# Optimization experiments

Measured on AMD Instinct MI355X. Metric: run time of the kernel, lower is better.

Reference implementation:

```python
import jax, jax.numpy as jnp
import numpy as np

P, M, DG, F, H, DH = 2000, 150, 2000, 256, 4, 64
N1, N2 = P + M, P + DG          # adj1 nodes (patient+med), adj2 nodes (patient+diag)
E1, E2, EGP, EGM = 137600, 256000, 64000, 4800
GNN_LAYERS = 2
SA_HID = 128


def setup_inputs() -> dict:
    key = jax.random.key(0)
    ks = jax.random.split(key, 32)
    ri = lambda k, n, hi: jax.random.randint(k, (n,), 0, hi, dtype=jnp.int32)
    rn = lambda k, shape, scale: (jax.random.normal(k, shape, dtype=jnp.float32) * scale)
    inp = {
        'adj1_rows': ri(ks[0], E1, N1), 'adj1_cols': ri(ks[1], E1, N1),
        'adj1_vals': jax.random.uniform(ks[2], (E1,), dtype=jnp.float32),
        'adj2_rows': ri(ks[3], E2, N2), 'adj2_cols': ri(ks[4], E2, N2),
        'adj2_vals': jax.random.uniform(ks[5], (E2,), dtype=jnp.float32),
        'g0_src': ri(ks[6], EGP, P), 'g0_dst': ri(ks[7], EGP, P),
        'g1_src': ri(ks[8], EGP, P), 'g1_dst': ri(ks[9], EGP, P),
        'g2_src': ri(ks[10], EGM, M), 'g2_dst': ri(ks[11], EGM, M),
        'g3_src': ri(ks[12], EGM, M), 'g3_dst': ri(ks[13], EGM, M),
        'keepRate': 1,
        # learned parameters (xavier-ish scales)
        'pEmbed': rn(ks[14], (P, F), 0.05),
        'mEmbed': rn(ks[15], (M, F), 0.05),
        'dEmbed': rn(ks[16], (DG, F), 0.05),
        'gat_W': rn(ks[17], (4, F, H * DH), (2.0 / (F + H * DH)) ** 0.5),
        'gat_al': rn(ks[18], (4, H, DH), 0.1),
        'gat_ar': rn(ks[19], (4, H, DH), 0.1),
        'gat_b': jnp.zeros((4, H * DH), dtype=jnp.float32),
        'sa_W1': rn(ks[20], (H * DH, SA_HID), (2.0 / (H * DH + SA_HID)) ** 0.5),
        'sa_b1': jnp.zeros((SA_HID,), dtype=jnp.float32),
        'sa_W2': rn(ks[21], (SA_HID, 1), 0.1),
        'out_W': rn(ks[22], (2 * F, M), (2.0 / (2 * F + M)) ** 0.5),
        'out_b': jnp.zeros((M,), dtype=jnp.float32),
    }
    return inp


def _spmm(rows, cols, vals, x, n):
    # sparse adj @ x via gather + segment_sum
    return jax.ops.segment_sum(vals[:, None] * x[cols], rows, num_segments=n)


def _seg_softmax(e, seg, n):
    m = jax.ops.segment_max(e, seg, num_segments=n)          # [n, H]
    ex = jnp.exp(e - m[seg])
    s = jax.ops.segment_sum(ex, seg, num_segments=n)
    return ex / (s[seg] + 1e-9)


def _gat(h, W, al, ar, b, src, dst, n):
    # DGL GATConv, feat/attn dropout = 0, negative_slope = 0.2, activation = elu
    feat = (h @ W).reshape(n, H, DH)                          # [n, H, DH]
    el = (feat * al[None]).sum(-1)                            # [n, H]
    er = (feat * ar[None]).sum(-1)
    e = jax.nn.leaky_relu(el[src] + er[dst], negative_slope=0.2)  # [E, H]
    alpha = _seg_softmax(e, dst, n)                           # softmax over in-edges per dst
    out = jax.ops.segment_sum(alpha[:, :, None] * feat[src], dst, num_segments=n)
    out = out + b.reshape(1, H, DH)
    return jax.nn.elu(out).reshape(n, H * DH)


def _sem_att(z, W1, b1, W2):
    # z: [N, K, F]; shared projection; beta over K meta-paths
    w = (jnp.tanh(z @ W1 + b1) @ W2).mean(0)                  # [K, 1]
    beta = jax.nn.softmax(w, axis=0)                          # [K, 1]
    return (beta[None] * z).sum(1)                            # [N, F]


def reference(adj1_rows, adj1_cols, adj1_vals, adj2_rows, adj2_cols, adj2_vals,
              g0_src, g0_dst, g1_src, g1_dst, g2_src, g2_dst, g3_src, g3_dst,
              keepRate, pEmbed, mEmbed, dEmbed, gat_W, gat_al, gat_ar, gat_b,
              sa_W1, sa_b1, sa_W2, out_W, out_b):
    embeds1 = jnp.concatenate([pEmbed, mEmbed], axis=0)       # [N1, F]
    embeds2 = jnp.concatenate([pEmbed, dEmbed], axis=0)       # [N2, F]
    lat1, lat2 = embeds1, embeds2
    acc1 = jnp.zeros_like(embeds1)
    acc2 = jnp.zeros_like(embeds2)
    for _ in range(GNN_LAYERS):
        lat1 = jax.nn.leaky_relu(_spmm(adj1_rows, adj1_cols, adj1_vals, lat1, N1), negative_slope=0.5)
        lat2 = jax.nn.leaky_relu(_spmm(adj2_rows, adj2_cols, adj2_vals, lat2, N2), negative_slope=0.5)
        acc1 = acc1 + lat1
        acc2 = acc2 + lat2
    p1, m_gcn = acc1[:P], acc1[P:]
    p2, d_gcn = acc2[:P], acc2[P:]

    e0 = _gat(p1, gat_W[0], gat_al[0], gat_ar[0], gat_b[0], g0_src, g0_dst, P)
    e1 = _gat(p2, gat_W[1], gat_al[1], gat_ar[1], gat_b[1], g1_src, g1_dst, P)
    e2 = _gat(m_gcn, gat_W[2], gat_al[2], gat_ar[2], gat_b[2], g2_src, g2_dst, M)
    e3 = _gat(m_gcn, gat_W[3], gat_al[3], gat_ar[3], gat_b[3], g3_src, g3_dst, M)

    patient = _sem_att(jnp.stack([e0, e1], axis=1), sa_W1, sa_b1, sa_W2)  # [P, F]
    med = _sem_att(jnp.stack([e2, e3], axis=1), sa_W1, sa_b1, sa_W2)      # [M, F]

    # broadcasted pairwise concat -> ReLU -> Linear -> sum over pairing axis
    pm = jnp.concatenate([
        jnp.broadcast_to(patient[:, None, :], (P, M, F)),
        jnp.broadcast_to(med[None, :, :], (P, M, F)),
    ], axis=-1).reshape(P * M, 2 * F)
    simi = (jax.nn.relu(pm) @ out_W + out_b).reshape(P, M, M)
    simi_pm = simi.sum(axis=1)                                # [P, M]
    return (simi_pm, d_gcn, med, m_gcn, patient)
```

## Files before the change

kernel.cpp:

```cpp
#include <hip/hip_runtime.h>
#include <cmath>
#include <cstdint>

constexpr int P  = 2000, M = 150, DG = 2000, F = 256, H = 4, DH = 64;
constexpr int N1 = P + M;
constexpr int N2 = P + DG;
constexpr int E1 = 137600, E2 = 256000, EGP = 64000, EGM = 4800;
constexpr int SA_HID = 128;

constexpr int HO1 = E1, HO2 = E1 + E2, HO3 = HO2 + EGP, HO4 = HO3 + EGP,
              HO5 = HO4 + EGM, HOE = HO5 + EGM;

constexpr int CAP_A = 160;
constexpr int CAP_G = 96;
constexpr int OVF_CAP = 4096;

__global__ __launch_bounds__(256) void k_build(
    const int* __restrict__ a1r, const int* __restrict__ a1c, const float* __restrict__ a1v,
    const int* __restrict__ a2r, const int* __restrict__ a2c, const float* __restrict__ a2v,
    const int* __restrict__ d0, const int* __restrict__ s0,
    const int* __restrict__ d1, const int* __restrict__ s1,
    const int* __restrict__ d2, const int* __restrict__ s2,
    const int* __restrict__ d3, const int* __restrict__ s3,
    int* cur1, uint2* ell1, int* cur2, uint2* ell2,
    int* cu0, unsigned* eg0, int* cu1, unsigned* eg1,
    int* cu2, unsigned* eg2, int* cu3, unsigned* eg3,
    int* __restrict__ ovf_n, int4* __restrict__ ovf) {
  int tid = blockIdx.x * 256 + threadIdx.x;
  int T = gridDim.x * 256;
  int seg[4], row[4]; unsigned p0[4], p1[4];
#pragma unroll
  for (int u = 0; u < 4; ++u) {
    int i = tid + u * T;
    seg[u] = -1;
    if (i < HOE) {
      if (i < HO1)      { seg[u] = 0; row[u] = a1r[i]; p0[u] = (unsigned)a1c[i]; p1[u] = __float_as_uint(a1v[i]); }
      else if (i < HO2) { int j = i - HO1; seg[u] = 1; row[u] = a2r[j]; p0[u] = (unsigned)a2c[j]; p1[u] = __float_as_uint(a2v[j]); }
      else if (i < HO3) { int j = i - HO2; seg[u] = 2; row[u] = d0[j]; p0[u] = (unsigned)s0[j]; }
      else if (i < HO4) { int j = i - HO3; seg[u] = 3; row[u] = d1[j]; p0[u] = (unsigned)s1[j]; }
      else if (i < HO5) { int j = i - HO4; seg[u] = 4; row[u] = d2[j]; p0[u] = (unsigned)s2[j]; }
      else              { int j = i - HO5; seg[u] = 5; row[u] = d3[j]; p0[u] = (unsigned)s3[j]; }
    }
  }
#pragma unroll
  for (int u = 0; u < 4; ++u) {
    int r = row[u];
    switch (seg[u]) {
      case 0: { int slot = atomicAdd(&cur1[r], 1);
        if (slot < CAP_A) ell1[(size_t)r * CAP_A + slot] = make_uint2(p0[u], p1[u]);
        else { int o = atomicAdd(&ovf_n[0], 1); if (o < OVF_CAP) ovf[0 * OVF_CAP + o] = make_int4(r, (int)p0[u], (int)p1[u], 0); } } break;
      case 1: { int slot = atomicAdd(&cur2[r], 1);
        if (slot < CAP_A) ell2[(size_t)r * CAP_A + slot] = make_uint2(p0[u], p1[u]);
        else { int o = atomicAdd(&ovf_n[1], 1); if (o < OVF_CAP) ovf[1 * OVF_CAP + o] = make_int4(r, (int)p0[u], (int)p1[u], 0); } } break;
      case 2: { int slot = atomicAdd(&cu0[r], 1);
        if (slot < CAP_G) eg0[(size_t)r * CAP_G + slot] = p0[u];
        else { int o = atomicAdd(&ovf_n[2], 1); if (o < OVF_CAP) ovf[2 * OVF_CAP + o] = make_int4(r, (int)p0[u], 0, 0); } } break;
      case 3: { int slot = atomicAdd(&cu1[r], 1);
        if (slot < CAP_G) eg1[(size_t)r * CAP_G + slot] = p0[u];
        else { int o = atomicAdd(&ovf_n[3], 1); if (o < OVF_CAP) ovf[3 * OVF_CAP + o] = make_int4(r, (int)p0[u], 0, 0); } } break;
      case 4: { int slot = atomicAdd(&cu2[r], 1);
        if (slot < CAP_G) eg2[(size_t)r * CAP_G + slot] = p0[u];
        else { int o = atomicAdd(&ovf_n[4], 1); if (o < OVF_CAP) ovf[4 * OVF_CAP + o] = make_int4(r, (int)p0[u], 0, 0); } } break;
      case 5: { int slot = atomicAdd(&cu3[r], 1);
        if (slot < CAP_G) eg3[(size_t)r * CAP_G + slot] = p0[u];
        else { int o = atomicAdd(&ovf_n[5], 1); if (o < OVF_CAP) ovf[5 * OVF_CAP + o] = make_int4(r, (int)p0[u], 0, 0); } } break;
      default: break;
    }
  }
}

template<int LAYER>
__global__ __launch_bounds__(256) void k_spmm(
    const int* __restrict__ cur1, const uint2* __restrict__ ell1,
    const int* __restrict__ cur2, const uint2* __restrict__ ell2,
    const int* __restrict__ ovf_n, const int4* __restrict__ ovf,
    const float* __restrict__ pE, const float* __restrict__ mE, const float* __restrict__ dE,
    float* __restrict__ lat1, float* __restrict__ lat2,
    float* __restrict__ acc1, float* __restrict__ acc2,
    float* __restrict__ out_mgcn, float* __restrict__ out_dgcn) {
  int gw = (blockIdx.x * 256 + threadIdx.x) >> 6;
  if (gw >= N1 + N2) return;
  int lane = threadIdx.x & 63;
  bool g2 = gw >= N1;
  int row = g2 ? gw - N1 : gw;
  const uint2* pe = (g2 ? ell2 : ell1) + (size_t)row * CAP_A;
  const float* latin = g2 ? lat2 : lat1;
  const float* tailE = g2 ? dE : mE;
  int deg = (g2 ? cur2 : cur1)[row];
  int dn = deg < CAP_A ? deg : CAP_A;
  int fo = lane << 2;
  float4 s = {0.f, 0.f, 0.f, 0.f};
  auto fetch = [&](int c) -> float4 {
    const float* b;
    if (LAYER == 1) b = (c < P) ? (pE + (size_t)c * F) : (tailE + (size_t)(c - P) * F);
    else            b = latin + (size_t)c * F;
    return *(const float4*)(b + fo);
  };
  int i = 0;
  for (; i + 8 <= dn; i += 8) {
    uint2 m[8]; float4 a[8];
#pragma unroll
    for (int u = 0; u < 8; ++u) m[u] = pe[i + u];
#pragma unroll
    for (int u = 0; u < 8; ++u) a[u] = fetch((int)m[u].x);
#pragma unroll
    for (int u = 0; u < 8; ++u) {
      float v = __uint_as_float(m[u].y);
      s.x += v * a[u].x; s.y += v * a[u].y; s.z += v * a[u].z; s.w += v * a[u].w;
    }
  }
  for (; i + 4 <= dn; i += 4) {
    uint2 m0 = pe[i], m1 = pe[i + 1], m2 = pe[i + 2], m3 = pe[i + 3];
    float v0 = __uint_as_float(m0.y), v1 = __uint_as_float(m1.y),
          v2 = __uint_as_float(m2.y), v3 = __uint_as_float(m3.y);
    float4 a0 = fetch((int)m0.x), a1 = fetch((int)m1.x),
           a2 = fetch((int)m2.x), a3 = fetch((int)m3.x);
    s.x += v0 * a0.x + v1 * a1.x + v2 * a2.x + v3 * a3.x;
    s.y += v0 * a0.y + v1 * a1.y + v2 * a2.y + v3 * a3.y;
    s.z += v0 * a0.z + v1 * a1.z + v2 * a2.z + v3 * a3.z;
    s.w += v0 * a0.w + v1 * a1.w + v2 * a2.w + v3 * a3.w;
  }
  for (; i < dn; ++i) {
    uint2 m = pe[i];
    float v = __uint_as_float(m.y);
    float4 a = fetch((int)m.x);
    s.x += v * a.x; s.y += v * a.y; s.z += v * a.z; s.w += v * a.w;
  }
  {
    int gi = g2 ? 1 : 0;
    int on = ovf_n[gi];
    if (on > 0) {
      const int4* ol = ovf + gi * OVF_CAP;
      for (int k = 0; k < on; ++k) {
        int4 e = ol[k];
        if (e.x == row) {
          float v = __int_as_float(e.z);
          float4 a = fetch(e.y);
          s.x += v * a.x; s.y += v * a.y; s.z += v * a.z; s.w += v * a.w;
        }
      }
    }
  }
  float4 l;
  l.x = s.x > 0.f ? s.x : 0.5f * s.x;
  l.y = s.y > 0.f ? s.y : 0.5f * s.y;
  l.z = s.z > 0.f ? s.z : 0.5f * s.z;
  l.w = s.w > 0.f ? s.w : 0.5f * s.w;
  if (LAYER == 1) {
    *(float4*)((g2 ? lat2 : lat1) + (size_t)row * F + fo) = l;
  } else {
    float4 b = *(const float4*)(latin + (size_t)row * F + fo);
    float4 a = {b.x + l.x, b.y + l.y, b.z + l.z, b.w + l.w};
    *(float4*)((g2 ? acc2 : acc1) + (size_t)row * F + fo) = a;
    if (row >= P)
      *(float4*)((g2 ? out_dgcn : out_mgcn) + (size_t)(row - P) * F + fo) = a;
  }
}

constexpr int FR  = 8;
constexpr int NB0 = (P + FR - 1) / FR;
constexpr int NB2 = (M + FR - 1) / FR;
constexpr int FEAT_BLOCKS = 2 * NB0 + 2 * NB2;

__global__ __launch_bounds__(256) void k_gat_feat_all(
    const float* __restrict__ acc1, const float* __restrict__ acc2,
    const float* __restrict__ gat_W, const float* __restrict__ gat_al,
    const float* __restrict__ gat_ar,
    float* __restrict__ f0, float* __restrict__ f1,
    float* __restrict__ f2, float* __restrict__ f3,
    float* __restrict__ el, float* __restrict__ er) {
  int b = blockIdx.x;
  int g, rb, n; const float* h; float* fout;
  if (b < NB0)            { g = 0; rb = b;              n = P; h = acc1; fout = f0; }
  else if (b < 2 * NB0)   { g = 1; rb = b - NB0;        n = P; h = acc2; fout = f1; }
  else if (b < 2*NB0+NB2) { g = 2; rb = b - 2 * NB0;    n = M; h = acc1 + (size_t)P * F; fout = f2; }
  else                    { g = 3; rb = b - 2*NB0 - NB2; n = M; h = acc1 + (size_t)P * F; fout = f3; }
  int elo = (g == 0) ? 0 : (g == 1) ? P * H : (g == 2) ? 2 * P * H : (2 * P + M) * H;
  const float* W = gat_W + (size_t)g * F * F;
  __shared__ float hs[FR][F];
  int t = threadIdx.x;
  int r0 = rb * FR;
  for (int q = t; q < FR * 64; q += 256) {
    int r = q >> 6, ln = q & 63;
    int row = r0 + r;
    float4 v = {0.f, 0.f, 0.f, 0.f};
    if (row < n) v = *(const float4*)(h + (size_t)row * F + (ln << 2));
    *(float4*)&hs[r][ln << 2] = v;
  }
  __syncthreads();
  float acc[FR];
#pragma unroll
  for (int r = 0; r < FR; ++r) acc[r] = 0.f;
  for (int k = 0; k < F; k += 4) {
    float w0 = W[(size_t)k * F + t],       w1 = W[(size_t)(k + 1) * F + t],
          w2 = W[(size_t)(k + 2) * F + t], w3 = W[(size_t)(k + 3) * F + t];
#pragma unroll
    for (int r = 0; r < FR; ++r) {
      float4 h4 = *(const float4*)&hs[r][k];
      acc[r] += h4.x * w0 + h4.y * w1 + h4.z * w2 + h4.w * w3;
    }
  }
  int head = t >> 6, d = t & 63;
  float av = gat_al[g * H * DH + head * DH + d];
  float rv = gat_ar[g * H * DH + head * DH + d];
#pragma unroll
  for (int r = 0; r < FR; ++r) {
    int row = r0 + r;
    if (row < n) {
      fout[(size_t)row * F + t] = acc[r];
      float cl = acc[r] * av, cr = acc[r] * rv;
      for (int o = 32; o > 0; o >>= 1) {
        cl += __shfl_down(cl, o, 64);
        cr += __shfl_down(cr, o, 64);
      }
      if (d == 0) { el[elo + row * H + head] = cl; er[elo + row * H + head] = cr; }
    }
  }
}

__global__ __launch_bounds__(256) void k_gat_agg_all(
    const int* __restrict__ cu0, const unsigned* __restrict__ eg0,
    const int* __restrict__ cu1, const unsigned* __restrict__ eg1,
    const int* __restrict__ cu2, const unsigned* __restrict__ eg2,
    const int* __restrict__ cu3, const unsigned* __restrict__ eg3,
    const int* __restrict__ ovf_n, const int4* __restrict__ ovf,
    const float* __restrict__ el, const float* __restrict__ er,
    const float* __restrict__ f0, const float* __restrict__ f1,
    const float* __restrict__ f2, const float* __restrict__ f3,
    const float* __restrict__ gat_b,
    float* __restrict__ e0, float* __restrict__ e1,
    float* __restrict__ e2, float* __restrict__ e3) {
  int gw = (blockIdx.x * 256 + threadIdx.x) >> 6;
  if (gw >= 2 * P + 2 * M) return;
  int lane = threadIdx.x & 63;
  int g, row; const int* cu; const unsigned* eg; const float* feat; float* out; int elo;
  if (gw < P)            { g = 0; row = gw;             cu = cu0; eg = eg0; feat = f0; out = e0; elo = 0; }
  else if (gw < 2 * P)   { g = 1; row = gw - P;         cu = cu1; eg = eg1; feat = f1; out = e1; elo = P * H; }
  else if (gw < 2*P + M) { g = 2; row = gw - 2 * P;     cu = cu2; eg = eg2; feat = f2; out = e2; elo = 2 * P * H; }
  else                   { g = 3; row = gw - 2 * P - M; cu = cu3; eg = eg3; feat = f3; out = e3; elo = (2 * P + M) * H; }
  int head = lane >> 4;
  int fo = lane << 2;
  const float* elb = el + elo;
  float erv = er[elo + row * H + head];
  int deg = cu[row];
  int dn = deg < CAP_G ? deg : CAP_G;
  const unsigned* ps = eg + (size_t)row * CAP_G;
  int on = ovf_n[2 + g];
  const int4* ol = ovf + (2 + g) * OVF_CAP;
  float mx = -3.4e38f;
  int i = 0;
  for (; i + 4 <= dn; i += 4) {
    int s0 = (int)ps[i], s1 = (int)ps[i + 1], s2 = (int)ps[i + 2], s3 = (int)ps[i + 3];
    float a = elb[s0 * H + head] + erv, b = elb[s1 * H + head] + erv,
          c = elb[s2 * H + head] + erv, d = elb[s3 * H + head] + erv;
    a = a > 0.f ? a : 0.2f * a; b = b > 0.f ? b : 0.2f * b;
    c = c > 0.f ? c : 0.2f * c; d = d > 0.f ? d : 0.2f * d;
    mx = fmaxf(mx, fmaxf(fmaxf(a, b), fmaxf(c, d)));
  }
  for (; i < dn; ++i) {
    float a = elb[(int)ps[i] * H + head] + erv;
    a = a > 0.f ? a : 0.2f * a;
    mx = fmaxf(mx, a);
  }
  if (on > 0) {
    for (int k = 0; k < on; ++k) {
      int4 e = ol[k];
      if (e.x == row) {
        float a = elb[e.y * H + head] + erv;
        a = a > 0.f ? a : 0.2f * a;
        mx = fmaxf(mx, a);
      }
    }
  }
  float ssum = 0.f;
  float4 acc = {0.f, 0.f, 0.f, 0.f};
  i = 0;
  for (; i + 2 <= dn; i += 2) {
    int s0 = (int)ps[i], s1 = (int)ps[i + 1];
    float a = elb[s0 * H + head] + erv; a = a > 0.f ? a : 0.2f * a;
    float b = elb[s1 * H + head] + erv; b = b > 0.f ? b : 0.2f * b;
    float x0 = expf(a - mx), x1 = expf(b - mx);
    float4 q0 = *(const float4*)(feat + (size_t)s0 * F + fo);
    float4 q1 = *(const float4*)(feat + (size_t)s1 * F + fo);
    ssum += x0 + x1;
    acc.x += x0 * q0.x + x1 * q1.x;
    acc.y += x0 * q0.y + x1 * q1.y;
    acc.z += x0 * q0.z + x1 * q1.z;
    acc.w += x0 * q0.w + x1 * q1.w;
  }
  for (; i < dn; ++i) {
    int s0 = (int)ps[i];
    float a = elb[s0 * H + head] + erv; a = a > 0.f ? a : 0.2f * a;
    float x0 = expf(a - mx);
    float4 q0 = *(const float4*)(feat + (size_t)s0 * F + fo);
    ssum += x0;
    acc.x += x0 * q0.x; acc.y += x0 * q0.y; acc.z += x0 * q0.z; acc.w += x0 * q0.w;
  }
  if (on > 0) {
    for (int k = 0; k < on; ++k) {
      int4 e = ol[k];
      if (e.x == row) {
        float a = elb[e.y * H + head] + erv; a = a > 0.f ? a : 0.2f * a;
        float x0 = expf(a - mx);
        float4 q0 = *(const float4*)(feat + (size_t)e.y * F + fo);
        ssum += x0;
        acc.x += x0 * q0.x; acc.y += x0 * q0.y; acc.z += x0 * q0.z; acc.w += x0 * q0.w;
      }
    }
  }
  float inv = 1.f / (ssum + 1e-9f);
  const float* bb = gat_b + g * F + fo;
  float4 v = {acc.x * inv + bb[0], acc.y * inv + bb[1],
              acc.z * inv + bb[2], acc.w * inv + bb[3]};
  v.x = v.x > 0.f ? v.x : expm1f(v.x);
  v.y = v.y > 0.f ? v.y : expm1f(v.y);
  v.z = v.z > 0.f ? v.z : expm1f(v.z);
  v.w = v.w > 0.f ? v.w : expm1f(v.w);
  *(float4*)(out + (size_t)row * F + fo) = v;
}

constexpr int SR  = 8;
constexpr int SB0 = (P + SR - 1) / SR;
constexpr int SB2 = (M + SR - 1) / SR;
constexpr int SEM_BLOCKS = 2 * SB0 + 2 * SB2;

__global__ __launch_bounds__(128) void k_sem_w_all(
    const float* __restrict__ e0, const float* __restrict__ e1,
    const float* __restrict__ e2, const float* __restrict__ e3,
    const float* __restrict__ W1, const float* __restrict__ b1,
    const float* __restrict__ W2, float* __restrict__ w) {
  int b = blockIdx.x;
  int zid, rb, n; const float* z;
  if (b < SB0)            { zid = 0; rb = b;             n = P; z = e0; }
  else if (b < 2 * SB0)   { zid = 1; rb = b - SB0;       n = P; z = e1; }
  else if (b < 2*SB0+SB2) { zid = 2; rb = b - 2 * SB0;   n = M; z = e2; }
  else                    { zid = 3; rb = b - 2*SB0-SB2; n = M; z = e3; }
  __shared__ float zs[SR][F];
  int t = threadIdx.x;
  int r0 = rb * SR;
  for (int q = t; q < SR * 64; q += 128) {
    int r = q >> 6, ln = q & 63;
    int row = r0 + r;
    float4 v = {0.f, 0.f, 0.f, 0.f};
    if (row < n) v = *(const float4*)(z + (size_t)row * F + (ln << 2));
    *(float4*)&zs[r][ln << 2] = v;
  }
  __syncthreads();
  float hid[SR];
#pragma unroll
  for (int r = 0; r < SR; ++r) hid[r] = b1[t];
  for (int k = 0; k < F; k += 4) {
    float w0 = W1[(size_t)k * SA_HID + t],       w1 = W1[(size_t)(k + 1) * SA_HID + t],
          w2 = W1[(size_t)(k + 2) * SA_HID + t], w3 = W1[(size_t)(k + 3) * SA_HID + t];
#pragma unroll
    for (int r = 0; r < SR; ++r) {
      float4 z4 = *(const float4*)&zs[r][k];
      hid[r] += z4.x * w0 + z4.y * w1 + z4.z * w2 + z4.w * w3;
    }
  }
  float w2v = W2[t];
  float local = 0.f;
  for (int r = 0; r < SR; ++r) {
    int row = r0 + r;
    if (row < n) local += tanhf(hid[r]) * w2v;
  }
  for (int o = 32; o > 0; o >>= 1) local += __shfl_down(local, o, 64);
  __shared__ float pp[2];
  if ((t & 63) == 0) pp[t >> 6] = local;
  __syncthreads();
  if (t == 0) atomicAdd(&w[zid], pp[0] + pp[1]);
}

__global__ __launch_bounds__(256) void k_med_cvec(
    const float* __restrict__ e2, const float* __restrict__ e3,
    const float* __restrict__ w, const float* __restrict__ outW,
    const float* __restrict__ outb,
    float* __restrict__ out_med, float* __restrict__ cbuf) {
  int t = threadIdx.x;
  float m0 = w[2] * (1.f / M), m1 = w[3] * (1.f / M);
  float mxv = fmaxf(m0, m1);
  float a0 = expf(m0 - mxv), a1 = expf(m1 - mxv);
  float sc = 1.f / (a0 + a1);
  a0 *= sc; a1 *= sc;
  float4 rs = {0.f, 0.f, 0.f, 0.f};
  for (int j = t; j < M * F / 4; j += 256) {
    float4 u0 = ((const float4*)e2)[j], u1 = ((const float4*)e3)[j];
    float4 r = {a0 * u0.x + a1 * u1.x, a0 * u0.y + a1 * u1.y,
                a0 * u0.z + a1 * u1.z, a0 * u0.w + a1 * u1.w};
    ((float4*)out_med)[j] = r;
    rs.x += r.x > 0.f ? r.x : 0.f;
    rs.y += r.y > 0.f ? r.y : 0.f;
    rs.z += r.z > 0.f ? r.z : 0.f;
    rs.w += r.w > 0.f ? r.w : 0.f;
  }
  __shared__ float4 sv4[4][64];
  sv4[t >> 6][t & 63] = rs;
  __syncthreads();
  __shared__ float sv[F];
  if (t < 64) {
    float4 a = sv4[0][t], b = sv4[1][t], c = sv4[2][t], d = sv4[3][t];
    sv[t * 4 + 0] = a.x + b.x + c.x + d.x;
    sv[t * 4 + 1] = a.y + b.y + c.y + d.y;
    sv[t * 4 + 2] = a.z + b.z + c.z + d.z;
    sv[t * 4 + 3] = a.w + b.w + c.w + d.w;
  }
  __syncthreads();
  if (t < M) {
    float cc = (float)M * outb[t];
    for (int f = 0; f < F; f += 4) {
      cc += sv[f]     * outW[(size_t)(F + f) * M + t]
          + sv[f + 1] * outW[(size_t)(F + f + 1) * M + t]
          + sv[f + 2] * outW[(size_t)(F + f + 2) * M + t]
          + sv[f + 3] * outW[(size_t)(F + f + 3) * M + t];
    }
    cbuf[t] = cc;
  }
}

constexpr int FIN_R = 8;
__global__ __launch_bounds__(256) void k_final(
    const float* __restrict__ e0, const float* __restrict__ e1,
    const float* __restrict__ w, const float* __restrict__ outW,
    const float* __restrict__ c,
    float* __restrict__ out_pat, float* __restrict__ simi) {
  float m0 = w[0] * (1.f / P), m1 = w[1] * (1.f / P);
  float mxv = fmaxf(m0, m1);
  float a0 = expf(m0 - mxv), a1 = expf(m1 - mxv);
  float sc = 1.f / (a0 + a1);
  a0 *= sc; a1 *= sc;
  __shared__ float psh[FIN_R][F];
  int t = threadIdx.x;
  int r0 = blockIdx.x * FIN_R;
  for (int q = t; q < FIN_R * 64; q += 256) {
    int r = q >> 6, ln = q & 63;
    size_t off = (size_t)(r0 + r) * F + (ln << 2);
    float4 u0 = *(const float4*)(e0 + off), u1 = *(const float4*)(e1 + off);
    float4 v = {a0 * u0.x + a1 * u1.x, a0 * u0.y + a1 * u1.y,
                a0 * u0.z + a1 * u1.z, a0 * u0.w + a1 * u1.w};
    *(float4*)(out_pat + off) = v;
    v.x = v.x > 0.f ? v.x : 0.f; v.y = v.y > 0.f ? v.y : 0.f;
    v.z = v.z > 0.f ? v.z : 0.f; v.w = v.w > 0.f ? v.w : 0.f;
    *(float4*)&psh[r][ln << 2] = v;
  }
  __syncthreads();
  if (t < M) {
    float acc[FIN_R];
#pragma unroll
    for (int r = 0; r < FIN_R; ++r) acc[r] = 0.f;
    for (int f = 0; f < F; f += 4) {
      float w0 = outW[(size_t)f * M + t],       w1 = outW[(size_t)(f + 1) * M + t],
            w2 = outW[(size_t)(f + 2) * M + t], w3 = outW[(size_t)(f + 3) * M + t];
#pragma unroll
      for (int r = 0; r < FIN_R; ++r) {
        float4 p4 = *(const float4*)&psh[r][f];
        acc[r] += p4.x * w0 + p4.y * w1 + p4.z * w2 + p4.w * w3;
      }
    }
    float cv = c[t];
    for (int r = 0; r < FIN_R; ++r)
      simi[(size_t)(r0 + r) * M + t] = (float)M * acc[r] + cv;
  }
}

extern "C" void kernel_launch(void* const* d_in, const int* in_sizes, int n_in,
                              void* d_out, int out_size, void* d_ws, size_t ws_size,
                              hipStream_t stream) {
  const int*   adj1_rows = (const int*)d_in[0];
  const int*   adj1_cols = (const int*)d_in[1];
  const float* adj1_vals = (const float*)d_in[2];
  const int*   adj2_rows = (const int*)d_in[3];
  const int*   adj2_cols = (const int*)d_in[4];
  const float* adj2_vals = (const float*)d_in[5];
  const int*   g0_src = (const int*)d_in[6];
  const int*   g0_dst = (const int*)d_in[7];
  const int*   g1_src = (const int*)d_in[8];
  const int*   g1_dst = (const int*)d_in[9];
  const int*   g2_src = (const int*)d_in[10];
  const int*   g2_dst = (const int*)d_in[11];
  const int*   g3_src = (const int*)d_in[12];
  const int*   g3_dst = (const int*)d_in[13];
  const float* pE     = (const float*)d_in[15];
  const float* mE     = (const float*)d_in[16];
  const float* dE     = (const float*)d_in[17];
  const float* gat_W  = (const float*)d_in[18];
  const float* gat_al = (const float*)d_in[19];
  const float* gat_ar = (const float*)d_in[20];
  const float* gat_b  = (const float*)d_in[21];
  const float* sa_W1  = (const float*)d_in[22];
  const float* sa_b1  = (const float*)d_in[23];
  const float* sa_W2  = (const float*)d_in[24];
  const float* out_W  = (const float*)d_in[25];
  const float* out_b  = (const float*)d_in[26];

  int* ip = (int*)d_ws;
  int* cur1 = ip; ip += N1;
  int* cur2 = ip; ip += N2;
  int* cu0  = ip; ip += P;
  int* cu1  = ip; ip += P;
  int* cu2  = ip; ip += M;
  int* cu3  = ip; ip += M;
  int* ovf_n = ip; ip += 6;
  float* wbuf = (float*)ip; ip += 4;
  size_t memset_bytes = (size_t)((char*)ip - (char*)d_ws);

  uintptr_t up = ((uintptr_t)ip + 15) & ~(uintptr_t)15;
  int4* ovf = (int4*)up;
  uint2* ell1 = (uint2*)(ovf + 6 * OVF_CAP);
  uint2* ell2 = ell1 + (size_t)N1 * CAP_A;
  unsigned* eg0 = (unsigned*)(ell2 + (size_t)N2 * CAP_A);
  unsigned* eg1 = eg0 + (size_t)P * CAP_G;
  unsigned* eg2 = eg1 + (size_t)P * CAP_G;
  unsigned* eg3 = eg2 + (size_t)M * CAP_G;
  float* fp = (float*)(eg3 + (size_t)M * CAP_G);
  float* lat1 = fp; fp += (size_t)N1 * F;
  float* lat2 = fp; fp += (size_t)N2 * F;
  float* acc1 = fp; fp += (size_t)N1 * F;
  float* acc2 = fp; fp += (size_t)N2 * F;
  float* f0   = fp; fp += (size_t)P * F;
  float* f1   = fp; fp += (size_t)P * F;
  float* f2   = fp; fp += (size_t)M * F;
  float* f3   = fp; fp += (size_t)M * F;
  float* el   = fp; fp += (size_t)(2 * P + 2 * M) * H;
  float* er   = fp; fp += (size_t)(2 * P + 2 * M) * H;
  float* e0b  = fp; fp += (size_t)P * F;
  float* e1b  = fp; fp += (size_t)P * F;
  float* e2b  = fp; fp += (size_t)M * F;
  float* e3b  = fp; fp += (size_t)M * F;
  float* cbuf = fp; fp += 256;

  float* out_simi = (float*)d_out;
  float* out_dgcn = out_simi + (size_t)P * M;
  float* out_med  = out_dgcn + (size_t)DG * F;
  float* out_mgcn = out_med  + (size_t)M * F;
  float* out_pat  = out_mgcn + (size_t)M * F;

  hipMemsetAsync(d_ws, 0, memset_bytes, stream);

  int eb = ((HOE + 3) / 4 + 255) / 256;
  k_build<<<eb, 256, 0, stream>>>(adj1_rows, adj1_cols, adj1_vals,
                                  adj2_rows, adj2_cols, adj2_vals,
                                  g0_dst, g0_src, g1_dst, g1_src,
                                  g2_dst, g2_src, g3_dst, g3_src,
                                  cur1, ell1, cur2, ell2,
                                  cu0, eg0, cu1, eg1, cu2, eg2, cu3, eg3,
                                  ovf_n, ovf);

  int sb = ((N1 + N2) * 64 + 255) / 256;
  k_spmm<1><<<sb, 256, 0, stream>>>(cur1, ell1, cur2, ell2, ovf_n, ovf, pE, mE, dE,
                                    lat1, lat2, acc1, acc2, out_mgcn, out_dgcn);
  k_spmm<2><<<sb, 256, 0, stream>>>(cur1, ell1, cur2, ell2, ovf_n, ovf, pE, mE, dE,
                                    lat1, lat2, acc1, acc2, out_mgcn, out_dgcn);

  k_gat_feat_all<<<FEAT_BLOCKS, 256, 0, stream>>>(acc1, acc2, gat_W, gat_al, gat_ar,
                                                  f0, f1, f2, f3, el, er);
  int ab = ((2 * P + 2 * M) * 64 + 255) / 256;
  k_gat_agg_all<<<ab, 256, 0, stream>>>(cu0, eg0, cu1, eg1, cu2, eg2, cu3, eg3,
                                        ovf_n, ovf, el, er, f0, f1, f2, f3, gat_b,
                                        e0b, e1b, e2b, e3b);

  k_sem_w_all<<<SEM_BLOCKS, 128, 0, stream>>>(e0b, e1b, e2b, e3b, sa_W1, sa_b1, sa_W2, wbuf);

  k_med_cvec<<<1, 256, 0, stream>>>(e2b, e3b, wbuf, out_W, out_b, out_med, cbuf);

  k_final<<<P / FIN_R, 256, 0, stream>>>(e0b, e1b, wbuf, out_W, cbuf, out_pat, out_simi);
}
```

Baseline: 325.0 us.

## Partition edge-list build by destination row across XCD-aligned block groups

The ELL/adjacency build kernel now assigns each group of blocks (selected by blockIdx mod 8) a contiguous destination-row range. Every block scans all edges but only inserts those whose row falls in its range. The intent is to keep the atomic counter updates and slot writes for a row range local to one XCD's L2 cache, reducing cross-die atomic contention. In exchange, each edge's row index is read eight times, and column/value loads are deferred until after the filter.

```diff
diff --git a/kernel.cpp b/kernel.cpp
--- a/kernel.cpp
+++ b/kernel.cpp
@@ -14,6 +14,12 @@
 constexpr int CAP_A = 160;
 constexpr int CAP_G = 96;
 constexpr int OVF_CAP = 4096;
+
+constexpr int NPP1 = (N1 + 7) / 8;
+constexpr int NPP2 = (N2 + 7) / 8;
+constexpr int NPPP = (P + 7) / 8;
+constexpr int NPPM = (M + 7) / 8;
+constexpr int BUILD_R = 64;
 
 __global__ __launch_bounds__(256) void k_build(
     const int* __restrict__ a1r, const int* __restrict__ a1c, const float* __restrict__ a1v,
@@ -26,45 +32,73 @@
     int* cu0, unsigned* eg0, int* cu1, unsigned* eg1,
     int* cu2, unsigned* eg2, int* cu3, unsigned* eg3,
     int* __restrict__ ovf_n, int4* __restrict__ ovf) {
-  int tid = blockIdx.x * 256 + threadIdx.x;
-  int T = gridDim.x * 256;
-  int seg[4], row[4]; unsigned p0[4], p1[4];
-#pragma unroll
-  for (int u = 0; u < 4; ++u) {
-    int i = tid + u * T;
-    seg[u] = -1;
-    if (i < HOE) {
-      if (i < HO1)      { seg[u] = 0; row[u] = a1r[i]; p0[u] = (unsigned)a1c[i]; p1[u] = __float_as_uint(a1v[i]); }
-      else if (i < HO2) { int j = i - HO1; seg[u] = 1; row[u] = a2r[j]; p0[u] = (unsigned)a2c[j]; p1[u] = __float_as_uint(a2v[j]); }
-      else if (i < HO3) { int j = i - HO2; seg[u] = 2; row[u] = d0[j]; p0[u] = (unsigned)s0[j]; }
-      else if (i < HO4) { int j = i - HO3; seg[u] = 3; row[u] = d1[j]; p0[u] = (unsigned)s1[j]; }
-      else if (i < HO5) { int j = i - HO4; seg[u] = 4; row[u] = d2[j]; p0[u] = (unsigned)s2[j]; }
-      else              { int j = i - HO5; seg[u] = 5; row[u] = d3[j]; p0[u] = (unsigned)s3[j]; }
-    }
-  }
-#pragma unroll
-  for (int u = 0; u < 4; ++u) {
-    int r = row[u];
-    switch (seg[u]) {
-      case 0: { int slot = atomicAdd(&cur1[r], 1);
-        if (slot < CAP_A) ell1[(size_t)r * CAP_A + slot] = make_uint2(p0[u], p1[u]);
-        else { int o = atomicAdd(&ovf_n[0], 1); if (o < OVF_CAP) ovf[0 * OVF_CAP + o] = make_int4(r, (int)p0[u], (int)p1[u], 0); } } break;
-      case 1: { int slot = atomicAdd(&cur2[r], 1);
-        if (slot < CAP_A) ell2[(size_t)r * CAP_A + slot] = make_uint2(p0[u], p1[u]);
-        else { int o = atomicAdd(&ovf_n[1], 1); if (o < OVF_CAP) ovf[1 * OVF_CAP + o] = make_int4(r, (int)p0[u], (int)p1[u], 0); } } break;
-      case 2: { int slot = atomicAdd(&cu0[r], 1);
-        if (slot < CAP_G) eg0[(size_t)r * CAP_G + slot] = p0[u];
-        else { int o = atomicAdd(&ovf_n[2], 1); if (o < OVF_CAP) ovf[2 * OVF_CAP + o] = make_int4(r, (int)p0[u], 0, 0); } } break;
-      case 3: { int slot = atomicAdd(&cu1[r], 1);
-        if (slot < CAP_G) eg1[(size_t)r * CAP_G + slot] = p0[u];
-        else { int o = atomicAdd(&ovf_n[3], 1); if (o < OVF_CAP) ovf[3 * OVF_CAP + o] = make_int4(r, (int)p0[u], 0, 0); } } break;
-      case 4: { int slot = atomicAdd(&cu2[r], 1);
-        if (slot < CAP_G) eg2[(size_t)r * CAP_G + slot] = p0[u];
-        else { int o = atomicAdd(&ovf_n[4], 1); if (o < OVF_CAP) ovf[4 * OVF_CAP + o] = make_int4(r, (int)p0[u], 0, 0); } } break;
-      case 5: { int slot = atomicAdd(&cu3[r], 1);
-        if (slot < CAP_G) eg3[(size_t)r * CAP_G + slot] = p0[u];
-        else { int o = atomicAdd(&ovf_n[5], 1); if (o < OVF_CAP) ovf[5 * OVF_CAP + o] = make_int4(r, (int)p0[u], 0, 0); } } break;
-      default: break;
+  const int p = blockIdx.x & 7;
+  const int rank = blockIdx.x >> 3;
+  const int S = BUILD_R * 256;
+  const int lo1 = p * NPP1, hi1 = min(N1, lo1 + NPP1);
+  const int lo2 = p * NPP2, hi2 = min(N2, lo2 + NPP2);
+  const int loP = p * NPPP, hiP = min(P,  loP + NPPP);
+  const int loM = p * NPPM, hiM = min(M,  loM + NPPM);
+
+  for (int base = rank * 256 + (int)threadIdx.x; base < HOE; base += 4 * S) {
+    int idx[4], seg[4], row[4];
+    bool ok[4];
+#pragma unroll
+    for (int u = 0; u < 4; ++u) {
+      int i = base + u * S;
+      idx[u] = i; seg[u] = -1; ok[u] = false;
+      if (i < HOE) {
+        if (i < HO1)      { seg[u] = 0; row[u] = a1r[i];
+                            ok[u] = (row[u] >= lo1) & (row[u] < hi1); }
+        else if (i < HO2) { seg[u] = 1; row[u] = a2r[i - HO1];
+                            ok[u] = (row[u] >= lo2) & (row[u] < hi2); }
+        else if (i < HO3) { seg[u] = 2; row[u] = d0[i - HO2];
+                            ok[u] = (row[u] >= loP) & (row[u] < hiP); }
+        else if (i < HO4) { seg[u] = 3; row[u] = d1[i - HO3];
+                            ok[u] = (row[u] >= loP) & (row[u] < hiP); }
+        else if (i < HO5) { seg[u] = 4; row[u] = d2[i - HO4];
+                            ok[u] = (row[u] >= loM) & (row[u] < hiM); }
+        else              { seg[u] = 5; row[u] = d3[i - HO5];
+                            ok[u] = (row[u] >= loM) & (row[u] < hiM); }
+      }
+    }
+#pragma unroll
+    for (int u = 0; u < 4; ++u) {
+      if (!ok[u]) continue;
+      int r = row[u];
+      switch (seg[u]) {
+        case 0: { int i = idx[u];
+          int slot = atomicAdd(&cur1[r], 1);
+          unsigned c = (unsigned)a1c[i], v = __float_as_uint(a1v[i]);
+          if (slot < CAP_A) ell1[(size_t)r * CAP_A + slot] = make_uint2(c, v);
+          else { int o = atomicAdd(&ovf_n[0], 1); if (o < OVF_CAP) ovf[0 * OVF_CAP + o] = make_int4(r, (int)c, (int)v, 0); } } break;
+        case 1: { int j = idx[u] - HO1;
+          int slot = atomicAdd(&cur2[r], 1);
+          unsigned c = (unsigned)a2c[j], v = __float_as_uint(a2v[j]);
+          if (slot < CAP_A) ell2[(size_t)r * CAP_A + slot] = make_uint2(c, v);
+          else { int o = atomicAdd(&ovf_n[1], 1); if (o < OVF_CAP) ovf[1 * OVF_CAP + o] = make_int4(r, (int)c, (int)v, 0); } } break;
+        case 2: { int j = idx[u] - HO2;
+          int slot = atomicAdd(&cu0[r], 1);
+          unsigned sv = (unsigned)s0[j];
+          if (slot < CAP_G) eg0[(size_t)r * CAP_G + slot] = sv;
+          else { int o = atomicAdd(&ovf_n[2], 1); if (o < OVF_CAP) ovf[2 * OVF_CAP + o] = make_int4(r, (int)sv, 0, 0); } } break;
+        case 3: { int j = idx[u] - HO3;
+          int slot = atomicAdd(&cu1[r], 1);
+          unsigned sv = (unsigned)s1[j];
+          if (slot < CAP_G) eg1[(size_t)r * CAP_G + slot] = sv;
+          else { int o = atomicAdd(&ovf_n[3], 1); if (o < OVF_CAP) ovf[3 * OVF_CAP + o] = make_int4(r, (int)sv, 0, 0); } } break;
+        case 4: { int j = idx[u] - HO4;
+          int slot = atomicAdd(&cu2[r], 1);
+          unsigned sv = (unsigned)s2[j];
+          if (slot < CAP_G) eg2[(size_t)r * CAP_G + slot] = sv;
+          else { int o = atomicAdd(&ovf_n[4], 1); if (o < OVF_CAP) ovf[4 * OVF_CAP + o] = make_int4(r, (int)sv, 0, 0); } } break;
+        case 5: { int j = idx[u] - HO5;
+          int slot = atomicAdd(&cu3[r], 1);
+          unsigned sv = (unsigned)s3[j];
+          if (slot < CAP_G) eg3[(size_t)r * CAP_G + slot] = sv;
+          else { int o = atomicAdd(&ovf_n[5], 1); if (o < OVF_CAP) ovf[5 * OVF_CAP + o] = make_int4(r, (int)sv, 0, 0); } } break;
+        default: break;
+      }
     }
   }
 }
@@ -536,14 +570,13 @@
 
   hipMemsetAsync(d_ws, 0, memset_bytes, stream);
 
-  int eb = ((HOE + 3) / 4 + 255) / 256;
-  k_build<<<eb, 256, 0, stream>>>(adj1_rows, adj1_cols, adj1_vals,
-                                  adj2_rows, adj2_cols, adj2_vals,
-                                  g0_dst, g0_src, g1_dst, g1_src,
-                                  g2_dst, g2_src, g3_dst, g3_src,
-                                  cur1, ell1, cur2, ell2,
-                                  cu0, eg0, cu1, eg1, cu2, eg2, cu3, eg3,
-                                  ovf_n, ovf);
+  k_build<<<8 * BUILD_R, 256, 0, stream>>>(adj1_rows, adj1_cols, adj1_vals,
+                                           adj2_rows, adj2_cols, adj2_vals,
+                                           g0_dst, g0_src, g1_dst, g1_src,
+                                           g2_dst, g2_src, g3_dst, g3_src,
+                                           cur1, ell1, cur2, ell2,
+                                           cu0, eg0, cu1, eg1, cu2, eg2, cu3, eg3,
+                                           ovf_n, ovf);
 
   int sb = ((N1 + N2) * 64 + 255) / 256;
   k_spmm<1><<<sb, 256, 0, stream>>>(cur1, ell1, cur2, ell2, ovf_n, ovf, pE, mE, dE,
```

Result: slower. 361.3 us (+11.2%).
